# Kernel tuning notes

Measured on AMD Instinct MI355X. Metric: run time of the kernel, lower is better.

## Reference

```python
import jax, jax.numpy as jnp
import numpy as np

KQ = 512
NEG = -1e9


def setup_inputs() -> dict:
    key = jax.random.key(0)
    k1, k2, k3, k4, k5 = jax.random.split(key, 5)
    B, NQ, NK, D, V, O = 16, 1024, 2048, 512, 512, 256
    return {
        "keys": jax.random.normal(k1, (B, NK, D), dtype=jnp.float32),
        "queries": jax.random.normal(k2, (B, NQ, D), dtype=jnp.float32),
        "values": jax.random.normal(k3, (B, NK, V), dtype=jnp.float32),
        "mask": jax.random.randint(k4, (B, NQ, NK), 0, 2, dtype=jnp.int32),
        "W_resize": jax.random.normal(k5, (O, V), dtype=jnp.float32) * (1.0 / np.sqrt(V)),
        "b_resize": jnp.zeros((O,), dtype=jnp.float32),
    }


def reference(keys, queries, values, mask, W_resize, b_resize):
    # score: scaled dot product  [B, NQ, NK]
    logits = jnp.einsum("bqd,bkd->bqk", queries, keys) / jnp.sqrt(jnp.float32(KQ))
    logits = jnp.where(mask == 0, jnp.float32(NEG), logits)
    attn = jax.nn.softmax(logits, axis=-1)
    # context: [B, NQ, V]
    context = jnp.einsum("bqk,bkv->bqv", attn, values)
    # resize to out_size
    context = jnp.einsum("bqv,ov->bqo", context, W_resize) + b_resize
    return context
```

## Files before the change

kernel.cpp:

```cpp
#include <hip/hip_runtime.h>

#define BB   16
#define NQ   1024
#define NK   2048
#define DD   512
#define VV   512
#define OO   256
#define SCALE 0.044194173824159216f

typedef __attribute__((ext_vector_type(4))) float f32x4;
typedef __attribute__((ext_vector_type(8))) short s16x8;

#define AS1(p) ((const __attribute__((address_space(1))) void*)(p))
#define AS3(p) ((__attribute__((address_space(3))) void*)(p))

__device__ __forceinline__ unsigned short f2bf(float f) {
  unsigned u = __float_as_uint(f);
  u += 0x7fffu + ((u >> 16) & 1u);
  return (unsigned short)(u >> 16);
}
__device__ __forceinline__ float bf2f(unsigned short b) {
  return __uint_as_float(((unsigned)b) << 16);
}

__device__ __forceinline__ void gemm_bt_core(
    const unsigned short* __restrict__ Abase,
    const unsigned short* __restrict__ Bbase,
    int K,
    unsigned short* As, unsigned short* Bs,
    f32x4 acc[4][4])
{
  const int t = threadIdx.x;
  const int w = t >> 6;
  const int l = t & 63;
  const int srow = l >> 2;
  const int scol = (l & 3) * 8;
  const int r0 = (w * 2 + 0) * 16 + srow;
  const int r1 = (w * 2 + 1) * 16 + srow;
  const int lds0 = (w * 2 + 0) * 512 + l * 8;
  const int lds1 = (w * 2 + 1) * 512 + l * 8;
  const int wm = (w >> 1) * 64;
  const int wn = (w & 1) * 64;
  const int lm = l & 15;
  const int lq = l >> 4;

  for (int kt = 0; kt < K; kt += 32) {
    __builtin_amdgcn_global_load_lds(AS1(Abase + (size_t)r0 * K + kt + scol), AS3(As + lds0), 16, 0, 0);
    __builtin_amdgcn_global_load_lds(AS1(Abase + (size_t)r1 * K + kt + scol), AS3(As + lds1), 16, 0, 0);
    __builtin_amdgcn_global_load_lds(AS1(Bbase + (size_t)r0 * K + kt + scol), AS3(Bs + lds0), 16, 0, 0);
    __builtin_amdgcn_global_load_lds(AS1(Bbase + (size_t)r1 * K + kt + scol), AS3(Bs + lds1), 16, 0, 0);
    __syncthreads();
    s16x8 af[4], bfr[4];
    #pragma unroll
    for (int i = 0; i < 4; ++i) {
      af[i]  = *(const s16x8*)(As + (wm + i * 16 + lm) * 32 + lq * 8);
      bfr[i] = *(const s16x8*)(Bs + (wn + i * 16 + lm) * 32 + lq * 8);
    }
    #pragma unroll
    for (int mi = 0; mi < 4; ++mi)
      #pragma unroll
      for (int ni = 0; ni < 4; ++ni)
        acc[mi][ni] = __builtin_amdgcn_mfma_f32_16x16x32_bf16(af[mi], bfr[ni], acc[mi][ni], 0, 0, 0);
    __syncthreads();
  }
}


__global__ __launch_bounds__(256)
void qk_kernel(const unsigned short* __restrict__ Qb,
               const unsigned short* __restrict__ Kb,
               const int* __restrict__ mask,
               unsigned short* __restrict__ S)
{
  const int b  = blockIdx.z;
  const int tm = blockIdx.y;
  const int tn = blockIdx.x;
  __shared__ unsigned short As[128 * 32];
  __shared__ unsigned short Bs[128 * 32];
  f32x4 acc[4][4];
  #pragma unroll
  for (int i = 0; i < 4; ++i)
    #pragma unroll
    for (int j = 0; j < 4; ++j) acc[i][j] = (f32x4){0.f, 0.f, 0.f, 0.f};

  const unsigned short* Abase = Qb + ((size_t)b * NQ + tm * 128) * DD;
  const unsigned short* Bbase = Kb + ((size_t)b * NK + tn * 128) * DD;
  gemm_bt_core(Abase, Bbase, DD, As, Bs, acc);

  const int t = threadIdx.x, w = t >> 6, l = t & 63;
  const int wm = (w >> 1) * 64, wn = (w & 1) * 64;
  const int lm = l & 15, lq = l >> 4;
  #pragma unroll
  for (int mi = 0; mi < 4; ++mi)
    #pragma unroll
    for (int ni = 0; ni < 4; ++ni)
      #pragma unroll
      for (int r = 0; r < 4; ++r) {
        const int gq = tm * 128 + wm + mi * 16 + lq * 4 + r;
        const int gk = tn * 128 + wn + ni * 16 + lm;
        const size_t idx = ((size_t)b * NQ + gq) * NK + gk;
        float v = acc[mi][ni][r] * SCALE;
        v = mask[idx] ? v : -1e9f;
        S[idx] = f2bf(v);
      }
}

__global__ __launch_bounds__(256)
void softmax_kernel(unsigned short* __restrict__ S)
{
  const size_t row = blockIdx.x;
  unsigned short* p = S + row * NK;
  const int t = threadIdx.x, w = t >> 6, l = t & 63;
  __shared__ float sm[4];
  __shared__ float ss[4];

  s16x8 v = ((const s16x8*)p)[t];
  float x[8];
  #pragma unroll
  for (int j = 0; j < 8; ++j) x[j] = bf2f((unsigned short)v[j]);

  float mx = x[0];
  #pragma unroll
  for (int j = 1; j < 8; ++j) mx = fmaxf(mx, x[j]);
  #pragma unroll
  for (int off = 32; off > 0; off >>= 1) mx = fmaxf(mx, __shfl_down(mx, off, 64));
  if (l == 0) sm[w] = mx;
  __syncthreads();
  const float bm = fmaxf(fmaxf(sm[0], sm[1]), fmaxf(sm[2], sm[3]));

  float e[8], s = 0.f;
  #pragma unroll
  for (int j = 0; j < 8; ++j) { e[j] = __expf(x[j] - bm); s += e[j]; }
  #pragma unroll
  for (int off = 32; off > 0; off >>= 1) s += __shfl_down(s, off, 64);
  if (l == 0) ss[w] = s;
  __syncthreads();
  const float inv = 1.f / (ss[0] + ss[1] + ss[2] + ss[3]);

  s16x8 o;
  #pragma unroll
  for (int j = 0; j < 8; ++j) o[j] = (short)f2bf(e[j] * inv);
  ((s16x8*)p)[t] = o;
}

__global__ __launch_bounds__(256)
void pv_kernel(const unsigned short* __restrict__ P,
               const unsigned short* __restrict__ Vt,
               unsigned short* __restrict__ Ctx)
{
  const int b  = blockIdx.z;
  const int tm = blockIdx.y;
  const int tn = blockIdx.x;
  __shared__ unsigned short As[128 * 32];
  __shared__ unsigned short Bs[128 * 32];
  f32x4 acc[4][4];
  #pragma unroll
  for (int i = 0; i < 4; ++i)
    #pragma unroll
    for (int j = 0; j < 4; ++j) acc[i][j] = (f32x4){0.f, 0.f, 0.f, 0.f};

  const unsigned short* Abase = P  + ((size_t)b * NQ + tm * 128) * NK;
  const unsigned short* Bbase = Vt + ((size_t)b * VV + tn * 128) * NK;
  gemm_bt_core(Abase, Bbase, NK, As, Bs, acc);

  const int t = threadIdx.x, w = t >> 6, l = t & 63;
  const int wm = (w >> 1) * 64, wn = (w & 1) * 64;
  const int lm = l & 15, lq = l >> 4;
  #pragma unroll
  for (int mi = 0; mi < 4; ++mi)
    #pragma unroll
    for (int ni = 0; ni < 4; ++ni)
      #pragma unroll
      for (int r = 0; r < 4; ++r) {
        const int gq = tm * 128 + wm + mi * 16 + lq * 4 + r;
        const int gv = tn * 128 + wn + ni * 16 + lm;
        Ctx[((size_t)b * NQ + gq) * VV + gv] = f2bf(acc[mi][ni][r]);
      }
}

__global__ __launch_bounds__(256)
void rs_kernel(const unsigned short* __restrict__ Ctx,
               const unsigned short* __restrict__ Wb,
               const float* __restrict__ bias,
               float* __restrict__ out)
{
  const int tm = blockIdx.y;
  const int tn = blockIdx.x;
  __shared__ unsigned short As[128 * 32];
  __shared__ unsigned short Bs[128 * 32];
  f32x4 acc[4][4];
  #pragma unroll
  for (int i = 0; i < 4; ++i)
    #pragma unroll
    for (int j = 0; j < 4; ++j) acc[i][j] = (f32x4){0.f, 0.f, 0.f, 0.f};

  const unsigned short* Abase = Ctx + (size_t)tm * 128 * VV;
  const unsigned short* Bbase = Wb + (size_t)tn * 128 * VV;
  gemm_bt_core(Abase, Bbase, VV, As, Bs, acc);

  const int t = threadIdx.x, w = t >> 6, l = t & 63;
  const int wm = (w >> 1) * 64, wn = (w & 1) * 64;
  const int lm = l & 15, lq = l >> 4;
  #pragma unroll
  for (int mi = 0; mi < 4; ++mi)
    #pragma unroll
    for (int ni = 0; ni < 4; ++ni)
      #pragma unroll
      for (int r = 0; r < 4; ++r) {
        const int gm = tm * 128 + wm + mi * 16 + lq * 4 + r;
        const int gn = tn * 128 + wn + ni * 16 + lm;
        out[(size_t)gm * OO + gn] = acc[mi][ni][r] + bias[gn];
      }
}

__global__ __launch_bounds__(256)
void cvt_kernel(const float* __restrict__ in, unsigned short* __restrict__ out, int n8)
{
  const int i = blockIdx.x * 256 + threadIdx.x;
  if (i >= n8) return;
  const float4* p = (const float4*)in + (size_t)i * 2;
  const float4 a = p[0], b = p[1];
  s16x8 o;
  o[0] = (short)f2bf(a.x); o[1] = (short)f2bf(a.y);
  o[2] = (short)f2bf(a.z); o[3] = (short)f2bf(a.w);
  o[4] = (short)f2bf(b.x); o[5] = (short)f2bf(b.y);
  o[6] = (short)f2bf(b.z); o[7] = (short)f2bf(b.w);
  ((s16x8*)out)[i] = o;
}

__global__ __launch_bounds__(256)
void vt_kernel(const float* __restrict__ V, unsigned short* __restrict__ Vt)
{
  const int b  = blockIdx.z;
  const int k0 = blockIdx.y * 32;
  const int v0 = blockIdx.x * 32;
  __shared__ float tile[32][33];
  const int tx = threadIdx.x & 31, ty = threadIdx.x >> 5;
  #pragma unroll
  for (int j = 0; j < 32; j += 8)
    tile[ty + j][tx] = V[((size_t)b * NK + k0 + ty + j) * VV + v0 + tx];
  __syncthreads();
  #pragma unroll
  for (int j = 0; j < 32; j += 8)
    Vt[((size_t)b * VV + v0 + ty + j) * NK + k0 + tx] = f2bf(tile[tx][ty + j]);
}

extern "C" void kernel_launch(void* const* d_in, const int* in_sizes, int n_in,
                              void* d_out, int out_size, void* d_ws, size_t ws_size,
                              hipStream_t stream)
{
  const float* keys    = (const float*)d_in[0];
  const float* queries = (const float*)d_in[1];
  const float* values  = (const float*)d_in[2];
  const int*   mask    = (const int*)  d_in[3];
  const float* W       = (const float*)d_in[4];
  const float* bias    = (const float*)d_in[5];
  float* out = (float*)d_out;

  char* ws = (char*)d_ws;
  unsigned short* Qb = (unsigned short*)(ws);
  unsigned short* Kb = (unsigned short*)(ws + (16ull << 20));
  unsigned short* Vt = (unsigned short*)(ws + (48ull << 20));
  unsigned short* Wb = (unsigned short*)(ws + (80ull << 20));
  unsigned short* S  = (unsigned short*)(ws + (81ull << 20));
  unsigned short* Ctx = Qb;

  cvt_kernel<<<dim3(4096), 256, 0, stream>>>(queries, Qb, (BB * NQ * DD) / 8);
  cvt_kernel<<<dim3(8192), 256, 0, stream>>>(keys, Kb, (BB * NK * DD) / 8);
  cvt_kernel<<<dim3(64),   256, 0, stream>>>(W, Wb, (OO * VV) / 8);
  vt_kernel<<<dim3(VV / 32, NK / 32, BB), 256, 0, stream>>>(values, Vt);

  qk_kernel<<<dim3(NK / 128, NQ / 128, BB), 256, 0, stream>>>(Qb, Kb, mask, S);
  softmax_kernel<<<dim3(BB * NQ), 256, 0, stream>>>(S);
  pv_kernel<<<dim3(VV / 128, NQ / 128, BB), 256, 0, stream>>>(S, Vt, Ctx);
  rs_kernel<<<dim3(OO / 128, (BB * NQ) / 128, 1), 256, 0, stream>>>(Ctx, Wb, bias, out);
}
```

Measured before the change: 481.2 us.

## Stage GEMM epilogues through LDS for vectorized stores; move mask to softmax

```diff
diff --git a/kernel.cpp b/kernel.cpp
--- a/kernel.cpp
+++ b/kernel.cpp
@@ -66,26 +66,28 @@
 }
 
 
+#define CS_STRIDE 136
+
 __global__ __launch_bounds__(256)
 void qk_kernel(const unsigned short* __restrict__ Qb,
                const unsigned short* __restrict__ Kb,
-               const int* __restrict__ mask,
                unsigned short* __restrict__ S)
 {
   const int b  = blockIdx.z;
   const int tm = blockIdx.y;
   const int tn = blockIdx.x;
-  __shared__ unsigned short As[128 * 32];
-  __shared__ unsigned short Bs[128 * 32];
+  __shared__ unsigned short smem[128 * CS_STRIDE];
+  unsigned short* As = smem;
+  unsigned short* Bs = smem + 4096;
+  unsigned short* Cs = smem;
   f32x4 acc[4][4];
   #pragma unroll
   for (int i = 0; i < 4; ++i)
     #pragma unroll
     for (int j = 0; j < 4; ++j) acc[i][j] = (f32x4){0.f, 0.f, 0.f, 0.f};
 
-  const unsigned short* Abase = Qb + ((size_t)b * NQ + tm * 128) * DD;
-  const unsigned short* Bbase = Kb + ((size_t)b * NK + tn * 128) * DD;
-  gemm_bt_core(Abase, Bbase, DD, As, Bs, acc);
+  gemm_bt_core(Qb + ((size_t)b * NQ + tm * 128) * DD,
+               Kb + ((size_t)b * NK + tn * 128) * DD, DD, As, Bs, acc);
 
   const int t = threadIdx.x, w = t >> 6, l = t & 63;
   const int wm = (w >> 1) * 64, wn = (w & 1) * 64;
@@ -95,29 +97,39 @@
     #pragma unroll
     for (int ni = 0; ni < 4; ++ni)
       #pragma unroll
-      for (int r = 0; r < 4; ++r) {
-        const int gq = tm * 128 + wm + mi * 16 + lq * 4 + r;
-        const int gk = tn * 128 + wn + ni * 16 + lm;
-        const size_t idx = ((size_t)b * NQ + gq) * NK + gk;
-        float v = acc[mi][ni][r] * SCALE;
-        v = mask[idx] ? v : -1e9f;
-        S[idx] = f2bf(v);
-      }
-}
-
-__global__ __launch_bounds__(256)
-void softmax_kernel(unsigned short* __restrict__ S)
+      for (int r = 0; r < 4; ++r)
+        Cs[(wm + mi * 16 + lq * 4 + r) * CS_STRIDE + wn + ni * 16 + lm] =
+            f2bf(acc[mi][ni][r] * SCALE);
+  __syncthreads();
+  const int trow = t >> 4, tcol = (t & 15) * 8;
+  #pragma unroll
+  for (int it = 0; it < 8; ++it) {
+    const int row = it * 16 + trow;
+    s16x8 v = *(const s16x8*)(Cs + row * CS_STRIDE + tcol);
+    *(s16x8*)(S + ((size_t)b * NQ + tm * 128 + row) * NK + tn * 128 + tcol) = v;
+  }
+}
+
+__global__ __launch_bounds__(256)
+void softmax_kernel(unsigned short* __restrict__ S, const int* __restrict__ mask)
 {
   const size_t row = blockIdx.x;
   unsigned short* p = S + row * NK;
+  const int* mrow = mask + row * NK;
   const int t = threadIdx.x, w = t >> 6, l = t & 63;
   __shared__ float sm[4];
   __shared__ float ss[4];
 
+  const int4 m0 = ((const int4*)mrow)[t * 2];
+  const int4 m1 = ((const int4*)mrow)[t * 2 + 1];
   s16x8 v = ((const s16x8*)p)[t];
   float x[8];
   #pragma unroll
   for (int j = 0; j < 8; ++j) x[j] = bf2f((unsigned short)v[j]);
+  x[0] = m0.x ? x[0] : -1e9f;  x[1] = m0.y ? x[1] : -1e9f;
+  x[2] = m0.z ? x[2] : -1e9f;  x[3] = m0.w ? x[3] : -1e9f;
+  x[4] = m1.x ? x[4] : -1e9f;  x[5] = m1.y ? x[5] : -1e9f;
+  x[6] = m1.z ? x[6] : -1e9f;  x[7] = m1.w ? x[7] : -1e9f;
 
   float mx = x[0];
   #pragma unroll
@@ -151,17 +163,18 @@
   const int b  = blockIdx.z;
   const int tm = blockIdx.y;
   const int tn = blockIdx.x;
-  __shared__ unsigned short As[128 * 32];
-  __shared__ unsigned short Bs[128 * 32];
+  __shared__ unsigned short smem[128 * CS_STRIDE];
+  unsigned short* As = smem;
+  unsigned short* Bs = smem + 4096;
+  unsigned short* Cs = smem;
   f32x4 acc[4][4];
   #pragma unroll
   for (int i = 0; i < 4; ++i)
     #pragma unroll
     for (int j = 0; j < 4; ++j) acc[i][j] = (f32x4){0.f, 0.f, 0.f, 0.f};
 
-  const unsigned short* Abase = P  + ((size_t)b * NQ + tm * 128) * NK;
-  const unsigned short* Bbase = Vt + ((size_t)b * VV + tn * 128) * NK;
-  gemm_bt_core(Abase, Bbase, NK, As, Bs, acc);
+  gemm_bt_core(P  + ((size_t)b * NQ + tm * 128) * NK,
+               Vt + ((size_t)b * VV + tn * 128) * NK, NK, As, Bs, acc);
 
   const int t = threadIdx.x, w = t >> 6, l = t & 63;
   const int wm = (w >> 1) * 64, wn = (w & 1) * 64;
@@ -171,13 +184,20 @@
     #pragma unroll
     for (int ni = 0; ni < 4; ++ni)
       #pragma unroll
-      for (int r = 0; r < 4; ++r) {
-        const int gq = tm * 128 + wm + mi * 16 + lq * 4 + r;
-        const int gv = tn * 128 + wn + ni * 16 + lm;
-        Ctx[((size_t)b * NQ + gq) * VV + gv] = f2bf(acc[mi][ni][r]);
-      }
-}
-
+      for (int r = 0; r < 4; ++r)
+        Cs[(wm + mi * 16 + lq * 4 + r) * CS_STRIDE + wn + ni * 16 + lm] =
+            f2bf(acc[mi][ni][r]);
+  __syncthreads();
+  const int trow = t >> 4, tcol = (t & 15) * 8;
+  #pragma unroll
+  for (int it = 0; it < 8; ++it) {
+    const int row = it * 16 + trow;
+    s16x8 v = *(const s16x8*)(Cs + row * CS_STRIDE + tcol);
+    *(s16x8*)(Ctx + ((size_t)b * NQ + tm * 128 + row) * VV + tn * 128 + tcol) = v;
+  }
+}
+
+#define CSF_STRIDE 136
 __global__ __launch_bounds__(256)
 void rs_kernel(const unsigned short* __restrict__ Ctx,
                const unsigned short* __restrict__ Wb,
@@ -186,17 +206,18 @@
 {
   const int tm = blockIdx.y;
   const int tn = blockIdx.x;
-  __shared__ unsigned short As[128 * 32];
-  __shared__ unsigned short Bs[128 * 32];
+  __shared__ float smemf[128 * CSF_STRIDE];
+  unsigned short* As = (unsigned short*)smemf;
+  unsigned short* Bs = (unsigned short*)smemf + 4096;
+  float* Cs = smemf;
   f32x4 acc[4][4];
   #pragma unroll
   for (int i = 0; i < 4; ++i)
     #pragma unroll
     for (int j = 0; j < 4; ++j) acc[i][j] = (f32x4){0.f, 0.f, 0.f, 0.f};
 
-  const unsigned short* Abase = Ctx + (size_t)tm * 128 * VV;
-  const unsigned short* Bbase = Wb + (size_t)tn * 128 * VV;
-  gemm_bt_core(Abase, Bbase, VV, As, Bs, acc);
+  gemm_bt_core(Ctx + (size_t)tm * 128 * VV,
+               Wb + (size_t)tn * 128 * VV, VV, As, Bs, acc);
 
   const int t = threadIdx.x, w = t >> 6, l = t & 63;
   const int wm = (w >> 1) * 64, wn = (w & 1) * 64;
@@ -206,11 +227,23 @@
     #pragma unroll
     for (int ni = 0; ni < 4; ++ni)
       #pragma unroll
-      for (int r = 0; r < 4; ++r) {
-        const int gm = tm * 128 + wm + mi * 16 + lq * 4 + r;
-        const int gn = tn * 128 + wn + ni * 16 + lm;
-        out[(size_t)gm * OO + gn] = acc[mi][ni][r] + bias[gn];
-      }
+      for (int r = 0; r < 4; ++r)
+        Cs[(wm + mi * 16 + lq * 4 + r) * CSF_STRIDE + wn + ni * 16 + lm] = acc[mi][ni][r];
+  __syncthreads();
+  const int trow = t >> 4, tcol = (t & 15) * 8;
+  #pragma unroll
+  for (int it = 0; it < 8; ++it) {
+    const int row = it * 16 + trow;
+    f32x4 a = *(const f32x4*)(Cs + row * CSF_STRIDE + tcol);
+    f32x4 c = *(const f32x4*)(Cs + row * CSF_STRIDE + tcol + 4);
+    const int gn = tn * 128 + tcol;
+    const f32x4 b0 = *(const f32x4*)(bias + gn);
+    const f32x4 b1 = *(const f32x4*)(bias + gn + 4);
+    a += b0; c += b1;
+    float* o = out + (size_t)(tm * 128 + row) * OO + gn;
+    *(f32x4*)o = a;
+    *(f32x4*)(o + 4) = c;
+  }
 }
 
 __global__ __launch_bounds__(256)
@@ -228,21 +261,32 @@
   ((s16x8*)out)[i] = o;
 }
 
+#define VT_STRIDE 68
 __global__ __launch_bounds__(256)
 void vt_kernel(const float* __restrict__ V, unsigned short* __restrict__ Vt)
 {
   const int b  = blockIdx.z;
-  const int k0 = blockIdx.y * 32;
-  const int v0 = blockIdx.x * 32;
-  __shared__ float tile[32][33];
-  const int tx = threadIdx.x & 31, ty = threadIdx.x >> 5;
-  #pragma unroll
-  for (int j = 0; j < 32; j += 8)
-    tile[ty + j][tx] = V[((size_t)b * NK + k0 + ty + j) * VV + v0 + tx];
-  __syncthreads();
-  #pragma unroll
-  for (int j = 0; j < 32; j += 8)
-    Vt[((size_t)b * VV + v0 + ty + j) * NK + k0 + tx] = f2bf(tile[tx][ty + j]);
+  const int k0 = blockIdx.y * 64;
+  const int v0 = blockIdx.x * 64;
+  __shared__ float tile[64 * VT_STRIDE];
+  const int t = threadIdx.x;
+  const int lr = t >> 4, lc4 = (t & 15) * 4;
+  #pragma unroll
+  for (int j = 0; j < 4; ++j) {
+    const int row = lr + j * 16;
+    const float4 x = *(const float4*)(V + ((size_t)b * NK + k0 + row) * VV + v0 + lc4);
+    *(float4*)(tile + row * VT_STRIDE + lc4) = x;
+  }
+  __syncthreads();
+  const int vr = t >> 3, kx = (t & 7) * 8;
+  #pragma unroll
+  for (int j = 0; j < 2; ++j) {
+    const int v = vr + j * 32;
+    s16x8 o;
+    #pragma unroll
+    for (int i = 0; i < 8; ++i) o[i] = (short)f2bf(tile[(kx + i) * VT_STRIDE + v]);
+    *(s16x8*)(Vt + ((size_t)b * VV + v0 + v) * NK + k0 + kx) = o;
+  }
 }
 
 extern "C" void kernel_launch(void* const* d_in, const int* in_sizes, int n_in,
@@ -268,10 +312,10 @@
   cvt_kernel<<<dim3(4096), 256, 0, stream>>>(queries, Qb, (BB * NQ * DD) / 8);
   cvt_kernel<<<dim3(8192), 256, 0, stream>>>(keys, Kb, (BB * NK * DD) / 8);
   cvt_kernel<<<dim3(64),   256, 0, stream>>>(W, Wb, (OO * VV) / 8);
-  vt_kernel<<<dim3(VV / 32, NK / 32, BB), 256, 0, stream>>>(values, Vt);
-
-  qk_kernel<<<dim3(NK / 128, NQ / 128, BB), 256, 0, stream>>>(Qb, Kb, mask, S);
-  softmax_kernel<<<dim3(BB * NQ), 256, 0, stream>>>(S);
+  vt_kernel<<<dim3(VV / 64, NK / 64, BB), 256, 0, stream>>>(values, Vt);
+
+  qk_kernel<<<dim3(NK / 128, NQ / 128, BB), 256, 0, stream>>>(Qb, Kb, S);
+  softmax_kernel<<<dim3(BB * NQ), 256, 0, stream>>>(S, mask);
   pv_kernel<<<dim3(VV / 128, NQ / 128, BB), 256, 0, stream>>>(S, Vt, Ctx);
   rs_kernel<<<dim3(OO / 128, (BB * NQ) / 128, 1), 256, 0, stream>>>(Ctx, Wb, bias, out);
 }
```

Result: faster. 464.7 us (-3.4%).
